# Kernel optimization log

Measured on AMD Instinct MI355X. Metric: run time of the kernel, lower is better.

The kernel has to match this reference:

```python
import jax, jax.numpy as jnp
import numpy as np

K = 3          # up_k
EPS = 1e-8
BN_EPS = 1e-5
NEG_SLOPE = 0.2


def _knn(dense_xyz, sparse_xyz, k):
    # dense_xyz: (B,3,N), sparse_xyz: (B,3,S) -> squared dists (B,N,k), idx (B,N,k)
    inner = jnp.einsum('bcn,bcs->bns', dense_xyz, sparse_xyz)
    n2 = jnp.sum(dense_xyz * dense_xyz, axis=1)   # (B,N)
    s2 = jnp.sum(sparse_xyz * sparse_xyz, axis=1)  # (B,S)
    d2 = n2[:, :, None] + s2[:, None, :] - 2.0 * inner  # (B,N,S)
    d2 = jnp.maximum(d2, 0.0)
    neg_d, idx = jax.lax.top_k(-d2, k)  # k smallest distances
    return -neg_d, idx


def setup_inputs() -> dict:
    key = jax.random.key(0)
    ks = jax.random.split(key, 7)
    B, N, S = 4, 16384, 4096
    Cd, Cs = 128, 256           # dense / sparse feature channels (Cd + Cs = 3*v_dense)
    Co = 128                    # v_dense
    return {
        'dense_points_xyz': jax.random.normal(ks[0], (B, 3, N), jnp.float32),
        'sparse_points_xyz': jax.random.normal(ks[1], (B, 3, S), jnp.float32),
        'dense_points_data': jax.random.normal(ks[2], (B, Cd, N), jnp.float32),
        'sparse_points_data': jax.random.normal(ks[3], (B, Cs, S), jnp.float32),
        'conv_w': jax.random.normal(ks[4], (Co, Cd + Cs), jnp.float32) * (1.0 / np.sqrt(Cd + Cs)),
        'bn_gamma': jnp.ones((Co,), jnp.float32),
        'bn_beta': jnp.zeros((Co,), jnp.float32),
    }


def reference(dense_points_xyz, sparse_points_xyz, dense_points_data,
              sparse_points_data, conv_w, bn_gamma, bn_beta):
    # ---- interpolate: KNN + inverse-distance weighted sum ----
    d, idx = _knn(dense_points_xyz, sparse_points_xyz, K)   # (B,N,K) each
    # gather sparse features: (B,Cs,S), idx (B,N,K) -> (B,Cs,N,K)
    neighbors = jax.vmap(lambda sd, ix: sd[:, ix])(sparse_points_data, idx)
    w = 1.0 / (d + EPS)
    w = w / jnp.sum(w, axis=-1, keepdims=True)              # (B,N,K)
    interp = jnp.sum(neighbors * w[:, None, :, :], axis=-1)  # (B,Cs,N)

    # ---- concat + 1x1 conv + BatchNorm (training-mode batch stats) + LeakyReLU ----
    x = jnp.concatenate([dense_points_data, interp], axis=1)  # (B, 3*v_dense, N)
    y = jnp.einsum('oc,bcn->bon', conv_w, x)                  # (B, v_dense, N)
    mean = jnp.mean(y, axis=(0, 2), keepdims=True)
    var = jnp.var(y, axis=(0, 2), keepdims=True)
    y = (y - mean) * jax.lax.rsqrt(var + BN_EPS)
    y = y * bn_gamma[None, :, None] + bn_beta[None, :, None]
    y = jnp.where(y >= 0, y, NEG_SLOPE * y)
    return y, dense_points_xyz
```

## Files before the change

### kernel.cpp

```cpp
#include <hip/hip_runtime.h>

constexpr int B  = 4;
constexpr int N  = 16384;
constexpr int S  = 4096;
constexpr int CD = 128;
constexpr int CS = 256;
constexpr int CO = 128;
constexpr int CIN = CD + CS;

constexpr int NC = 8;
constexpr int CH = S / NC;
constexpr int P  = 2;

__device__ __forceinline__ void insert3vi(float& d0, float& d1, float& d2,
                                          int& i0, int& i1, int& i2,
                                          float x, int sg) {
  const bool lt2 = x < d2;
  i2 = lt2 ? sg : i2;
  const bool lt1 = x < d1;
  i2 = lt1 ? i1 : i2;
  int i1t = lt1 ? sg : i1;
  const bool lt0 = x < d0;
  i1 = lt0 ? i0 : i1t;
  i0 = lt0 ? sg : i0;
  d2 = fminf(fmaxf(x, d1), d2);
  d1 = __builtin_amdgcn_fmed3f(x, d0, d1);
  d0 = fminf(x, d0);
}

__global__ __launch_bounds__(256) void knn_chunk_kernel(
    const float* __restrict__ dxyz, const float* __restrict__ sxyz,
    float* __restrict__ cdist, int* __restrict__ cidx) {
  __shared__ float4 sp[CH];
  const int b = blockIdx.z;
  const int c = blockIdx.y;
  const int nbase = blockIdx.x * (256 * P);
  const int t = threadIdx.x;

  const float* sb = sxyz + b * 3 * S + c * CH;
  for (int j = t; j < CH; j += 256) {
    const float sx = sb[j], sy = sb[S + j], sz = sb[2 * S + j];
    sp[j] = make_float4(-2.f * sx, -2.f * sy, -2.f * sz,
                        fmaf(sx, sx, fmaf(sy, sy, sz * sz)));
  }
  __syncthreads();

  float bx[P], by[P], bz[P];
  float d0[P], d1[P], d2[P];
  int   i0[P], i1[P], i2[P];
  #pragma unroll
  for (int p = 0; p < P; ++p) {
    const int n = nbase + p * 256 + t;
    bx[p] = dxyz[b * 3 * N + n];
    by[p] = dxyz[b * 3 * N + N + n];
    bz[p] = dxyz[b * 3 * N + 2 * N + n];
    d0[p] = d1[p] = d2[p] = 1e30f;
    i0[p] = i1[p] = i2[p] = 0;
  }

  #pragma unroll 4
  for (int j = 0; j < CH; ++j) {
    const float4 q = sp[j];
    const int sg = c * CH + j;
    #pragma unroll
    for (int p = 0; p < P; ++p) {
      const float x =
          fmaf(q.x, bx[p], fmaf(q.y, by[p], fmaf(q.z, bz[p], q.w)));
      insert3vi(d0[p], d1[p], d2[p], i0[p], i1[p], i2[p], x, sg);
    }
  }

  #pragma unroll
  for (int p = 0; p < P; ++p) {
    const int n = nbase + p * 256 + t;
    const size_t base = (((size_t)c * B + b) * N + n) * 3;
    cdist[base + 0] = d0[p]; cidx[base + 0] = i0[p];
    cdist[base + 1] = d1[p]; cidx[base + 1] = i1[p];
    cdist[base + 2] = d2[p]; cidx[base + 2] = i2[p];
  }
}

__global__ __launch_bounds__(256) void knn_merge_kernel(
    const float* __restrict__ cdist, const int* __restrict__ cidx,
    const float* __restrict__ dxyz, const float* __restrict__ sxyz,
    float* __restrict__ wgt, int* __restrict__ idx) {
  const int gid = blockIdx.x * 256 + threadIdx.x;
  const int b = gid >> 14;
  const int n = gid & (N - 1);
  float d0 = 1e30f, d1 = 1e30f, d2 = 1e30f;
  int i0 = 0, i1 = 0, i2 = 0;
  #pragma unroll
  for (int c = 0; c < NC; ++c) {
    const size_t base = ((size_t)c * B * N + gid) * 3;
    #pragma unroll
    for (int k = 0; k < 3; ++k) {
      insert3vi(d0, d1, d2, i0, i1, i2, cdist[base + k], cidx[base + k]);
    }
  }
  int ii[3] = {i0, i1, i2};

  const float bx = dxyz[b * 3 * N + n];
  const float by = dxyz[b * 3 * N + N + n];
  const float bz = dxyz[b * 3 * N + 2 * N + n];
  const float n2 = bx * bx + by * by + bz * bz;
  float w[3];
  #pragma unroll
  for (int k = 0; k < 3; ++k) {
    const float sx = sxyz[b * 3 * S + ii[k]];
    const float sy = sxyz[b * 3 * S + S + ii[k]];
    const float sz = sxyz[b * 3 * S + 2 * S + ii[k]];
    const float s2 = sx * sx + sy * sy + sz * sz;
    const float inner = bx * sx + by * sy + bz * sz;
    const float d = fmaxf((n2 + s2) - 2.f * inner, 0.f);
    w[k] = 1.f / (d + 1e-8f);
  }
  const float inv = 1.f / (w[0] + w[1] + w[2]);
  const size_t base = (size_t)gid * 3;
  wgt[base + 0] = w[0] * inv;
  wgt[base + 1] = w[1] * inv;
  wgt[base + 2] = w[2] * inv;
  idx[base + 0] = ii[0];
  idx[base + 1] = ii[1];
  idx[base + 2] = ii[2];
}

__global__ __launch_bounds__(256) void wtrans_kernel(
    const float* __restrict__ cw, float* __restrict__ wt) {
  const int i = blockIdx.x * 256 + threadIdx.x;
  const int o = i / CIN;
  const int c = i - o * CIN;
  wt[c * CO + o] = cw[i];
}

__global__ __launch_bounds__(64) void zproj_kernel(
    const float* __restrict__ sdata, const float* __restrict__ wt,
    float* __restrict__ Z) {
  const int b = blockIdx.z;
  const int og = blockIdx.y;
  const int s = blockIdx.x * 64 + threadIdx.x;
  const float* __restrict__ xp = sdata + b * CS * S + s;
  const float* __restrict__ wp = wt + CD * CO + og * 16;

  float acc[16];
  #pragma unroll
  for (int i = 0; i < 16; ++i) acc[i] = 0.f;

  #pragma unroll 4
  for (int c = 0; c < CS; ++c) {
    const float xv = xp[c * S];
    #pragma unroll
    for (int i = 0; i < 16; ++i)
      acc[i] = fmaf(wp[c * CO + i], xv, acc[i]);
  }

  float4* zp = reinterpret_cast<float4*>(Z + (b * S + s) * CO + og * 16);
  #pragma unroll
  for (int i = 0; i < 4; ++i)
    zp[i] = make_float4(acc[4*i+0], acc[4*i+1], acc[4*i+2], acc[4*i+3]);
}

__global__ __launch_bounds__(256) void ygemm_kernel(
    const float* __restrict__ ddata, const float* __restrict__ cw,
    const float* __restrict__ Z, const float* __restrict__ wgt,
    const int* __restrict__ idx, float* __restrict__ y) {
  const int b = blockIdx.y;
  const int n = blockIdx.x * 64 + (threadIdx.x & 63);
  const int rg = __builtin_amdgcn_readfirstlane(threadIdx.x >> 6);
  const float* __restrict__ xp = ddata + b * CD * N + n;
  const float* __restrict__ wp = cw + rg * 32 * CIN;

  float acc[32];
  #pragma unroll
  for (int i = 0; i < 32; ++i) acc[i] = 0.f;

  #pragma unroll 4
  for (int c = 0; c < CD; ++c) {
    const float xv = xp[c * N];
    #pragma unroll
    for (int i = 0; i < 32; ++i)
      acc[i] = fmaf(wp[i * CIN + c], xv, acc[i]);
  }

  const int pb = (b * N + n) * 3;
  #pragma unroll
  for (int k = 0; k < 3; ++k) {
    const float wk = wgt[pb + k];
    const int ik = idx[pb + k];
    const float4* zp =
        reinterpret_cast<const float4*>(Z + (b * S + ik) * CO + rg * 32);
    #pragma unroll
    for (int i = 0; i < 8; ++i) {
      float4 zv = zp[i];
      acc[4*i+0] = fmaf(wk, zv.x, acc[4*i+0]);
      acc[4*i+1] = fmaf(wk, zv.y, acc[4*i+1]);
      acc[4*i+2] = fmaf(wk, zv.z, acc[4*i+2]);
      acc[4*i+3] = fmaf(wk, zv.w, acc[4*i+3]);
    }
  }

  float* yp = y + b * CO * N + (rg * 32) * N + n;
  #pragma unroll
  for (int i = 0; i < 32; ++i) yp[i * N] = acc[i];
}

__global__ __launch_bounds__(256) void stats_kernel(
    const float* __restrict__ y, float* __restrict__ stats) {
  const int o = blockIdx.x;
  const int b = blockIdx.y;
  const float4* yp = reinterpret_cast<const float4*>(y + (b * CO + o) * N);
  float s = 0.f, sq = 0.f;
  for (int j = threadIdx.x; j < N / 4; j += 256) {
    float4 v = yp[j];
    s  += v.x + v.y + v.z + v.w;
    sq += v.x * v.x + v.y * v.y + v.z * v.z + v.w * v.w;
  }
  __shared__ float ls[256];
  __shared__ float lq[256];
  ls[threadIdx.x] = s;
  lq[threadIdx.x] = sq;
  __syncthreads();
  for (int st = 128; st > 0; st >>= 1) {
    if (threadIdx.x < (unsigned)st) {
      ls[threadIdx.x] += ls[threadIdx.x + st];
      lq[threadIdx.x] += lq[threadIdx.x + st];
    }
    __syncthreads();
  }
  if (threadIdx.x == 0) {
    atomicAdd(&stats[o], ls[0]);
    atomicAdd(&stats[CO + o], lq[0]);
  }
}

__global__ void scaleshift_kernel(const float* __restrict__ stats,
                                  const float* __restrict__ gamma,
                                  const float* __restrict__ beta,
                                  float* __restrict__ ss) {
  const int o = threadIdx.x;
  const float invc = 1.f / (float)(B * N);
  const float m = stats[o] * invc;
  float v = stats[CO + o] * invc - m * m;
  v = fmaxf(v, 0.f);
  const float sc = gamma[o] / sqrtf(v + 1e-5f);
  ss[o] = sc;
  ss[CO + o] = beta[o] - m * sc;
}

__global__ __launch_bounds__(256) void norm_kernel(float* __restrict__ y,
                                                   const float* __restrict__ ss) {
  const int i = blockIdx.x * 256 + threadIdx.x;
  const int o = (i >> 12) & (CO - 1);
  const float sc = ss[o];
  const float sh = ss[CO + o];
  float4* yp = reinterpret_cast<float4*>(y);
  float4 v = yp[i];
  float t;
  t = fmaf(v.x, sc, sh); v.x = fmaxf(t, 0.2f * t);
  t = fmaf(v.y, sc, sh); v.y = fmaxf(t, 0.2f * t);
  t = fmaf(v.z, sc, sh); v.z = fmaxf(t, 0.2f * t);
  t = fmaf(v.w, sc, sh); v.w = fmaxf(t, 0.2f * t);
  yp[i] = v;
}

extern "C" void kernel_launch(void* const* d_in, const int* in_sizes, int n_in,
                              void* d_out, int out_size, void* d_ws, size_t ws_size,
                              hipStream_t stream) {
  const float* dxyz  = (const float*)d_in[0];
  const float* sxyz  = (const float*)d_in[1];
  const float* ddata = (const float*)d_in[2];
  const float* sdata = (const float*)d_in[3];
  const float* cw    = (const float*)d_in[4];
  const float* gamma = (const float*)d_in[5];
  const float* beta  = (const float*)d_in[6];
  float* out = (float*)d_out;

  char* wsb = (char*)d_ws;
  float*  wgt  = (float*) (wsb);
  int*    idx  = (int*)   (wsb + 786432);
  float*  cdist= (float*) (wsb + 1572864);
  int*    cidx = (int*)   (wsb + 7864320);
  float*  Z    = (float*) (wsb + 1572864);
  float*  wt   = (float*) (wsb + 9961472);
  float*  stats= (float*) (wsb + 14155776);
  float*  ss   = (float*) (wsb + 14156800);

  hipMemsetAsync(stats, 0, 2 * CO * sizeof(float), stream);

  knn_chunk_kernel<<<dim3(N / (256 * P), NC, B), 256, 0, stream>>>(dxyz, sxyz, cdist, cidx);
  knn_merge_kernel<<<dim3(B * N / 256), 256, 0, stream>>>(cdist, cidx, dxyz, sxyz, wgt, idx);
  wtrans_kernel   <<<dim3(CO * CIN / 256), 256, 0, stream>>>(cw, wt);
  zproj_kernel    <<<dim3(S / 64, CO / 16, B), 64, 0, stream>>>(sdata, wt, Z);
  ygemm_kernel    <<<dim3(N / 64, B), 256, 0, stream>>>(ddata, cw, Z, wgt, idx, out);
  stats_kernel    <<<dim3(CO, B), 256, 0, stream>>>(out, stats);
  scaleshift_kernel<<<1, 128, 0, stream>>>(stats, gamma, beta, ss);
  norm_kernel     <<<(B * CO * N / 4) / 256, 256, 0, stream>>>(out, ss);

  hipMemcpyAsync(out + (size_t)B * CO * N, dxyz, (size_t)B * 3 * N * sizeof(float),
                 hipMemcpyDeviceToDevice, stream);
}
```

Baseline: 258.8 us.

## Replace brute-force KNN with uniform-grid spatial binning and shell search

Brute-force chunked KNN over all sparse points, plus its merge pass, is replaced by a 40^3 uniform grid. Sparse points are counted, prefix-scanned and scattered into cells. Each dense point then scans cells in growing cubic shells and stops early once the shell boundary exceeds the current third-best distance. This cuts the quadratic distance work, but adds several small kernels, serial scans, divergent per-thread loops and irregular memory access. The grid bounds assume roughly normal-distributed coordinates and clamp outliers into the edge cells.

Result: slower. 853.1 us (+229.7%).

```diff
diff --git a/kernel.cpp b/kernel.cpp
--- a/kernel.cpp
+++ b/kernel.cpp
@@ -8,101 +8,171 @@
 constexpr int CO = 128;
 constexpr int CIN = CD + CS;
 
-constexpr int NC = 8;
-constexpr int CH = S / NC;
-constexpr int P  = 2;
-
-__device__ __forceinline__ void insert3vi(float& d0, float& d1, float& d2,
-                                          int& i0, int& i1, int& i2,
-                                          float x, int sg) {
-  const bool lt2 = x < d2;
-  i2 = lt2 ? sg : i2;
-  const bool lt1 = x < d1;
-  i2 = lt1 ? i1 : i2;
-  int i1t = lt1 ? sg : i1;
-  const bool lt0 = x < d0;
-  i1 = lt0 ? i0 : i1t;
+constexpr int   G    = 40;
+constexpr int   G3   = G * G * G;
+constexpr float GLO  = -6.5f;
+constexpr float GH   = 13.0f / 40.0f;
+constexpr float GINV = 1.0f / GH;
+
+__device__ __forceinline__ int cell1(float x) {
+  int c = (int)floorf((x - GLO) * GINV);
+  return min(max(c, 0), G - 1);
+}
+
+__device__ __forceinline__ bool lex_lt(float x, int sg, float d, int i) {
+  return (x < d) | ((x == d) & (sg < i));
+}
+
+__device__ __forceinline__ void insert3lex(float& d0, float& d1, float& d2,
+                                           int& i0, int& i1, int& i2,
+                                           float x, int sg) {
+  const bool lt2 = lex_lt(x, sg, d2, i2);
+  const bool lt1 = lex_lt(x, sg, d1, i1);
+  const bool lt0 = lex_lt(x, sg, d0, i0);
+  i2 = lt1 ? i1 : (lt2 ? sg : i2);
+  i1 = lt0 ? i0 : (lt1 ? sg : i1);
   i0 = lt0 ? sg : i0;
   d2 = fminf(fmaxf(x, d1), d2);
   d1 = __builtin_amdgcn_fmed3f(x, d0, d1);
   d0 = fminf(x, d0);
 }
 
-__global__ __launch_bounds__(256) void knn_chunk_kernel(
+__global__ __launch_bounds__(256) void bin_count_kernel(
+    const float* __restrict__ sxyz, unsigned* __restrict__ cnt) {
+  const int gid = blockIdx.x * 256 + threadIdx.x;
+  const int b = gid >> 12;
+  const int s = gid & (S - 1);
+  const float sx = sxyz[b * 3 * S + s];
+  const float sy = sxyz[b * 3 * S + S + s];
+  const float sz = sxyz[b * 3 * S + 2 * S + s];
+  const int cid = (cell1(sz) * G + cell1(sy)) * G + cell1(sx);
+  atomicAdd(&cnt[b * G3 + cid], 1u);
+}
+
+constexpr int SCAN_T = 1024;
+constexpr int SCAN_C = (G3 + SCAN_T - 1) / SCAN_T;
+
+__global__ __launch_bounds__(1024) void bin_scan_kernel(
+    const unsigned* __restrict__ cnt, unsigned* __restrict__ ofs,
+    unsigned* __restrict__ cursor) {
+  const int b = blockIdx.x;
+  const int t = threadIdx.x;
+  const unsigned* C = cnt + b * G3;
+  unsigned* O = ofs + b * G3;
+  unsigned* U = cursor + b * G3;
+  const int lo = t * SCAN_C;
+  const int hi = min(lo + SCAN_C, G3);
+  unsigned mysum = 0;
+  for (int i = lo; i < hi; ++i) mysum += C[i];
+  __shared__ unsigned part[SCAN_T];
+  part[t] = mysum;
+  __syncthreads();
+  for (int off = 1; off < SCAN_T; off <<= 1) {
+    unsigned v = (t >= off) ? part[t - off] : 0u;
+    __syncthreads();
+    part[t] += v;
+    __syncthreads();
+  }
+  unsigned run = part[t] - mysum;
+  for (int i = lo; i < hi; ++i) {
+    O[i] = run;
+    U[i] = run;
+    run += C[i];
+  }
+}
+
+__global__ __launch_bounds__(256) void bin_scatter_kernel(
+    const float* __restrict__ sxyz, unsigned* __restrict__ cursor,
+    int* __restrict__ sortedS) {
+  const int gid = blockIdx.x * 256 + threadIdx.x;
+  const int b = gid >> 12;
+  const int s = gid & (S - 1);
+  const float sx = sxyz[b * 3 * S + s];
+  const float sy = sxyz[b * 3 * S + S + s];
+  const float sz = sxyz[b * 3 * S + 2 * S + s];
+  const int cid = (cell1(sz) * G + cell1(sy)) * G + cell1(sx);
+  const unsigned pos = atomicAdd(&cursor[b * G3 + cid], 1u);
+  sortedS[b * S + pos] = s;
+}
+
+__global__ __launch_bounds__(256) void fill_q_kernel(
+    const float* __restrict__ sxyz, const int* __restrict__ sortedS,
+    float4* __restrict__ sortedQ) {
+  const int gid = blockIdx.x * 256 + threadIdx.x;
+  const int b = gid >> 12;
+  const int s = sortedS[gid];
+  const float sx = sxyz[b * 3 * S + s];
+  const float sy = sxyz[b * 3 * S + S + s];
+  const float sz = sxyz[b * 3 * S + 2 * S + s];
+  sortedQ[gid] = make_float4(-2.f * sx, -2.f * sy, -2.f * sz,
+                             fmaf(sx, sx, fmaf(sy, sy, sz * sz)));
+}
+
+__global__ __launch_bounds__(64) void knn_bin_kernel(
     const float* __restrict__ dxyz, const float* __restrict__ sxyz,
-    float* __restrict__ cdist, int* __restrict__ cidx) {
-  __shared__ float4 sp[CH];
-  const int b = blockIdx.z;
-  const int c = blockIdx.y;
-  const int nbase = blockIdx.x * (256 * P);
-  const int t = threadIdx.x;
-
-  const float* sb = sxyz + b * 3 * S + c * CH;
-  for (int j = t; j < CH; j += 256) {
-    const float sx = sb[j], sy = sb[S + j], sz = sb[2 * S + j];
-    sp[j] = make_float4(-2.f * sx, -2.f * sy, -2.f * sz,
-                        fmaf(sx, sx, fmaf(sy, sy, sz * sz)));
-  }
-  __syncthreads();
-
-  float bx[P], by[P], bz[P];
-  float d0[P], d1[P], d2[P];
-  int   i0[P], i1[P], i2[P];
-  #pragma unroll
-  for (int p = 0; p < P; ++p) {
-    const int n = nbase + p * 256 + t;
-    bx[p] = dxyz[b * 3 * N + n];
-    by[p] = dxyz[b * 3 * N + N + n];
-    bz[p] = dxyz[b * 3 * N + 2 * N + n];
-    d0[p] = d1[p] = d2[p] = 1e30f;
-    i0[p] = i1[p] = i2[p] = 0;
-  }
-
-  #pragma unroll 4
-  for (int j = 0; j < CH; ++j) {
-    const float4 q = sp[j];
-    const int sg = c * CH + j;
-    #pragma unroll
-    for (int p = 0; p < P; ++p) {
-      const float x =
-          fmaf(q.x, bx[p], fmaf(q.y, by[p], fmaf(q.z, bz[p], q.w)));
-      insert3vi(d0[p], d1[p], d2[p], i0[p], i1[p], i2[p], x, sg);
-    }
-  }
-
-  #pragma unroll
-  for (int p = 0; p < P; ++p) {
-    const int n = nbase + p * 256 + t;
-    const size_t base = (((size_t)c * B + b) * N + n) * 3;
-    cdist[base + 0] = d0[p]; cidx[base + 0] = i0[p];
-    cdist[base + 1] = d1[p]; cidx[base + 1] = i1[p];
-    cdist[base + 2] = d2[p]; cidx[base + 2] = i2[p];
-  }
-}
-
-__global__ __launch_bounds__(256) void knn_merge_kernel(
-    const float* __restrict__ cdist, const int* __restrict__ cidx,
-    const float* __restrict__ dxyz, const float* __restrict__ sxyz,
+    const unsigned* __restrict__ ofs, const unsigned* __restrict__ cnt,
+    const int* __restrict__ sortedS, const float4* __restrict__ sortedQ,
     float* __restrict__ wgt, int* __restrict__ idx) {
-  const int gid = blockIdx.x * 256 + threadIdx.x;
+  const int gid = blockIdx.x * 64 + threadIdx.x;
   const int b = gid >> 14;
   const int n = gid & (N - 1);
-  float d0 = 1e30f, d1 = 1e30f, d2 = 1e30f;
-  int i0 = 0, i1 = 0, i2 = 0;
-  #pragma unroll
-  for (int c = 0; c < NC; ++c) {
-    const size_t base = ((size_t)c * B * N + gid) * 3;
-    #pragma unroll
-    for (int k = 0; k < 3; ++k) {
-      insert3vi(d0, d1, d2, i0, i1, i2, cdist[base + k], cidx[base + k]);
-    }
-  }
-  int ii[3] = {i0, i1, i2};
-
   const float bx = dxyz[b * 3 * N + n];
   const float by = dxyz[b * 3 * N + N + n];
   const float bz = dxyz[b * 3 * N + 2 * N + n];
   const float n2 = bx * bx + by * by + bz * bz;
+  const int cx = cell1(bx), cy = cell1(by), cz = cell1(bz);
+  const float fx = bx - (GLO + cx * GH);
+  const float fy = by - (GLO + cy * GH);
+  const float fz = bz - (GLO + cz * GH);
+  const float minf = fminf(fminf(fminf(fx, GH - fx), fminf(fy, GH - fy)),
+                           fminf(fz, GH - fz));
+
+  const unsigned* __restrict__ OFS = ofs + b * G3;
+  const unsigned* __restrict__ CNTp = cnt + b * G3;
+  const int* __restrict__ SS = sortedS + b * S;
+  const float4* __restrict__ Q = sortedQ + b * S;
+
+  float d0 = 1e30f, d1 = 1e30f, d2 = 1e30f;
+  int i0 = 0, i1 = 0, i2 = 0;
+
+#define VISIT(AZ, AY, AX)                                                   \
+  do {                                                                      \
+    const int cid = (((AZ)*G + (AY)) * G + (AX));                           \
+    const unsigned o0 = OFS[cid];                                           \
+    const unsigned cc = CNTp[cid];                                          \
+    for (unsigned k = 0; k < cc; ++k) {                                     \
+      const float4 q = Q[o0 + k];                                           \
+      const int sg = SS[o0 + k];                                            \
+      const float x = fmaf(q.x, bx, fmaf(q.y, by, fmaf(q.z, bz, q.w)));     \
+      insert3lex(d0, d1, d2, i0, i1, i2, x, sg);                            \
+    }                                                                       \
+  } while (0)
+
+  for (int r = 0; r < G; ++r) {
+    if (r >= 1 && d2 < 1e29f) {
+      const float bnd = fmaf((float)(r - 1), GH, minf);
+      const float lim = fmaf(d2 + n2, 1.001f, 1e-4f);
+      if (bnd * bnd > lim) break;
+    }
+    const int zlo = max(cz - r, 0), zhi = min(cz + r, G - 1);
+    for (int az = zlo; az <= zhi; ++az) {
+      const int adz = (az > cz) ? (az - cz) : (cz - az);
+      const int ylo = max(cy - r, 0), yhi = min(cy + r, G - 1);
+      for (int ay = ylo; ay <= yhi; ++ay) {
+        const int ady = max(adz, (ay > cy) ? (ay - cy) : (cy - ay));
+        if (ady == r) {
+          const int xlo = max(cx - r, 0), xhi = min(cx + r, G - 1);
+          for (int ax = xlo; ax <= xhi; ++ax) VISIT(az, ay, ax);
+        } else {
+          if (cx - r >= 0) VISIT(az, ay, cx - r);
+          if (cx + r < G)  VISIT(az, ay, cx + r);
+        }
+      }
+    }
+  }
+#undef VISIT
+
+  int ii[3] = {i0, i1, i2};
   float w[3];
   #pragma unroll
   for (int k = 0; k < 3; ++k) {
@@ -275,22 +345,31 @@
   float* out = (float*)d_out;
 
   char* wsb = (char*)d_ws;
-  float*  wgt  = (float*) (wsb);
-  int*    idx  = (int*)   (wsb + 786432);
-  float*  cdist= (float*) (wsb + 1572864);
-  int*    cidx = (int*)   (wsb + 7864320);
-  float*  Z    = (float*) (wsb + 1572864);
-  float*  wt   = (float*) (wsb + 9961472);
-  float*  stats= (float*) (wsb + 14155776);
-  float*  ss   = (float*) (wsb + 14156800);
+  float*    wgt     = (float*)   (wsb);
+  int*      idxb    = (int*)     (wsb + 786432);
+  float*    Z       = (float*)   (wsb + 1572864);
+  unsigned* cnt     = (unsigned*)(wsb + 1572864);
+  unsigned* ofs     = (unsigned*)(wsb + 2596864);
+  unsigned* cursor  = (unsigned*)(wsb + 3620864);
+  int*      sortedS = (int*)     (wsb + 4644864);
+  float4*   sortedQ = (float4*)  (wsb + 4710400);
+  float*    wt      = (float*)   (wsb + 9961472);
+  float*    stats   = (float*)   (wsb + 14155776);
+  float*    ss      = (float*)   (wsb + 14156800);
 
   hipMemsetAsync(stats, 0, 2 * CO * sizeof(float), stream);
-
-  knn_chunk_kernel<<<dim3(N / (256 * P), NC, B), 256, 0, stream>>>(dxyz, sxyz, cdist, cidx);
-  knn_merge_kernel<<<dim3(B * N / 256), 256, 0, stream>>>(cdist, cidx, dxyz, sxyz, wgt, idx);
-  wtrans_kernel   <<<dim3(CO * CIN / 256), 256, 0, stream>>>(cw, wt);
+  hipMemsetAsync(cnt, 0, (size_t)B * G3 * sizeof(unsigned), stream);
+
+  bin_count_kernel  <<<B * S / 256, 256, 0, stream>>>(sxyz, cnt);
+  bin_scan_kernel   <<<B, SCAN_T, 0, stream>>>(cnt, ofs, cursor);
+  bin_scatter_kernel<<<B * S / 256, 256, 0, stream>>>(sxyz, cursor, sortedS);
+  fill_q_kernel     <<<B * S / 256, 256, 0, stream>>>(sxyz, sortedS, sortedQ);
+  knn_bin_kernel    <<<B * N / 64, 64, 0, stream>>>(dxyz, sxyz, ofs, cnt,
+                                                    sortedS, sortedQ, wgt, idxb);
+
+  wtrans_kernel   <<<CO * CIN / 256, 256, 0, stream>>>(cw, wt);
   zproj_kernel    <<<dim3(S / 64, CO / 16, B), 64, 0, stream>>>(sdata, wt, Z);
-  ygemm_kernel    <<<dim3(N / 64, B), 256, 0, stream>>>(ddata, cw, Z, wgt, idx, out);
+  ygemm_kernel    <<<dim3(N / 64, B), 256, 0, stream>>>(ddata, cw, Z, wgt, idxb, out);
   stats_kernel    <<<dim3(CO, B), 256, 0, stream>>>(out, stats);
   scaleshift_kernel<<<1, 128, 0, stream>>>(stats, gamma, beta, ss);
   norm_kernel     <<<(B * CO * N / 4) / 256, 256, 0, stream>>>(out, ss);
```
